# Kernel tuning notes

Hardware: AMD Instinct MI355X
Metric: run time of the kernel (lower is better)

The kernel has to match this reference:

```python
import jax, jax.numpy as jnp
import numpy as np

B, D, H, W, C = 2, 16, 16, 16, 64
CBAR = 32


def setup_inputs() -> dict:
    key = jax.random.key(0)
    ks = jax.random.split(key, 6)
    x = jax.random.normal(ks[0], (B, D, H, W, C), dtype=jnp.float32)
    # 1x1x1 Conv3D == per-voxel linear over channels; scale for stable softmax
    Wf = jax.random.normal(ks[1], (C, CBAR), dtype=jnp.float32) / np.sqrt(C)
    Wg = jax.random.normal(ks[2], (C, CBAR), dtype=jnp.float32) / np.sqrt(C)
    Wh = jax.random.normal(ks[3], (C, CBAR), dtype=jnp.float32) / np.sqrt(C)
    Wo = jax.random.normal(ks[4], (CBAR, C), dtype=jnp.float32) / np.sqrt(CBAR)
    bf = jnp.zeros((CBAR,), jnp.float32)
    bg = jnp.zeros((CBAR,), jnp.float32)
    bh = jnp.zeros((CBAR,), jnp.float32)
    bo = jnp.zeros((C,), jnp.float32)
    gamma = jnp.ones((), jnp.float32)
    return {"x": x, "Wf": Wf, "bf": bf, "Wg": Wg, "bg": bg,
            "Wh": Wh, "bh": bh, "Wo": Wo, "bo": bo, "gamma": gamma}


def reference(x, Wf, bf, Wg, bg, Wh, bh, Wo, bo, gamma):
    b, d, h, w, c = x.shape
    n = d * h * w
    xf = x.reshape(b, n, c)                       # [B, N, C]
    f = xf @ Wf + bf                              # [B, N, cbar] (keys)
    g = xf @ Wg + bg                              # [B, N, cbar] (queries)
    hv = xf @ Wh + bh                             # [B, N, cbar] (values)
    s = jnp.einsum('bqc,bkc->bqk', g, f)          # [B, N, N]
    beta = jax.nn.softmax(s, axis=-1)
    bhv = jnp.einsum('bqk,bkc->bqc', beta, hv)    # [B, N, cbar]
    o = bhv @ Wo + bo                             # [B, N, C]
    out = xf + gamma * o
    return out.reshape(b, d, h, w, c)
```

## Files before the change

kernel.cpp:

```cpp
#include <hip/hip_runtime.h>
#include <hip/hip_bf16.h>

typedef short short8 __attribute__((ext_vector_type(8)));
typedef float f32x4 __attribute__((ext_vector_type(4)));

__device__ __forceinline__ float bf2f(unsigned short v) {
    unsigned int u = ((unsigned int)v) << 16;
    float f;
    __builtin_memcpy(&f, &u, 4);
    return f;
}

__device__ __forceinline__ unsigned short f2bf(float f) {
    unsigned int u;
    __builtin_memcpy(&u, &f, 4);
    u += 0x7fffu + ((u >> 16) & 1u);
    return (unsigned short)(u >> 16);
}

__device__ __forceinline__ unsigned int pack2(float a, float b) {
    return (unsigned int)f2bf(a) | ((unsigned int)f2bf(b) << 16);
}

__device__ __forceinline__ unsigned int pack_trunc(float a, float b) {
    unsigned int ua, ub;
    __builtin_memcpy(&ua, &a, 4);
    __builtin_memcpy(&ub, &b, 4);
    return __builtin_amdgcn_perm(ub, ua, 0x07060302u);
}

__device__ __forceinline__ void split2(float a, float b,
                                       unsigned int& hi, unsigned int& lo) {
    unsigned short ah = f2bf(a), bh = f2bf(b);
    float al = a - bf2f(ah), bl = b - bf2f(bh);
    hi = (unsigned int)ah | ((unsigned int)bh << 16);
    lo = (unsigned int)f2bf(al) | ((unsigned int)f2bf(bl) << 16);
}

__device__ __forceinline__ float loadv(const void* p, int idx, bool is_fp32) {
    return is_fp32 ? ((const float*)p)[idx] : bf2f(((const unsigned short*)p)[idx]);
}
__device__ __forceinline__ bool detect_fp32(const void* x, int tid, int* flag_sh) {
    if (tid < 64) {
        unsigned int w = ((const unsigned int*)x)[tid];
        unsigned int e = (w >> 7) & 0xFFu;
        unsigned long long m = __ballot(e > 140u);
        if (tid == 0) *flag_sh = (__popcll(m) >= 8) ? 1 : 0;
    }
    __syncthreads();
    return *flag_sh != 0;
}

__global__ __launch_bounds__(128) void proj_kernel(
    const void* __restrict__ x,
    const void* __restrict__ Wf, const void* __restrict__ bfv,
    const void* __restrict__ Wg, const void* __restrict__ bgv,
    const void* __restrict__ Wh, const void* __restrict__ bhv,
    unsigned short* __restrict__ F, unsigned short* __restrict__ G,
    unsigned short* __restrict__ Ht) {
    __shared__ unsigned int WTh[3 * 32 * 36];
    __shared__ unsigned int WTl[3 * 32 * 36];
    __shared__ float bL[96];
    __shared__ int dflag;
    int tid = threadIdx.x;
    bool fp32 = detect_fp32(x, tid, &dflag);
    int lane = tid & 63, wave = tid >> 6;
    int Q = lane >> 4, l15 = lane & 15;
    int row0 = (blockIdx.x * 2 + wave) << 4;

    const void* Ws[3] = {Wf, Wg, Wh};
    const void* bs[3] = {bfv, bgv, bhv};

    for (int i = tid; i < 3072; i += 128) {
        int m = i >> 10;
        int r = i & 1023;
        int p = r >> 5, n = r & 31;
        float e0 = loadv(Ws[m], (2 * p) * 32 + n, fp32);
        float e1 = loadv(Ws[m], (2 * p + 1) * 32 + n, fp32);
        unsigned int hi, lo;
        split2(e0, e1, hi, lo);
        WTh[(m * 32 + n) * 36 + p] = hi;
        WTl[(m * 32 + n) * 36 + p] = lo;
    }
    if (tid < 96) bL[tid] = loadv(bs[tid >> 5], tid & 31, fp32);

    short8 a0h, a0l, a1h, a1l;
    {
        int base = (row0 + l15) * 64 + Q * 8;
        union { unsigned int u[4]; short8 s8; } A0h, A0l, A1h, A1l;
        if (fp32) {
            const float* xf = (const float*)x;
            f32x4 v0 = *(const f32x4*)(xf + base);
            f32x4 v1 = *(const f32x4*)(xf + base + 4);
            f32x4 w0 = *(const f32x4*)(xf + base + 32);
            f32x4 w1 = *(const f32x4*)(xf + base + 36);
            split2(v0[0], v0[1], A0h.u[0], A0l.u[0]);
            split2(v0[2], v0[3], A0h.u[1], A0l.u[1]);
            split2(v1[0], v1[1], A0h.u[2], A0l.u[2]);
            split2(v1[2], v1[3], A0h.u[3], A0l.u[3]);
            split2(w0[0], w0[1], A1h.u[0], A1l.u[0]);
            split2(w0[2], w0[3], A1h.u[1], A1l.u[1]);
            split2(w1[0], w1[1], A1h.u[2], A1l.u[2]);
            split2(w1[2], w1[3], A1h.u[3], A1l.u[3]);
        } else {
            const unsigned short* xb = (const unsigned short*)x;
            A0h.s8 = *(const short8*)(xb + base);
            A1h.s8 = *(const short8*)(xb + base + 32);
            A0l.u[0] = A0l.u[1] = A0l.u[2] = A0l.u[3] = 0;
            A1l = A0l;
        }
        a0h = A0h.s8; a0l = A0l.s8; a1h = A1h.s8; a1l = A1l.s8;
    }
    __syncthreads();

#pragma unroll
    for (int m = 0; m < 3; m++) {
#pragma unroll
        for (int cb = 0; cb < 2; cb++) {
            int rowbase = (m * 32 + cb * 16 + l15) * 36;
            union { uint4 v; short8 s8; } B0h, B0l, B1h, B1l;
            B0h.v = *(const uint4*)&WTh[rowbase + Q * 4];
            B1h.v = *(const uint4*)&WTh[rowbase + 16 + Q * 4];
            B0l.v = *(const uint4*)&WTl[rowbase + Q * 4];
            B1l.v = *(const uint4*)&WTl[rowbase + 16 + Q * 4];
            f32x4 z = {0.f, 0.f, 0.f, 0.f};
            f32x4 acc = __builtin_amdgcn_mfma_f32_16x16x32_bf16(a0h, B0h.s8, z, 0, 0, 0);
            acc = __builtin_amdgcn_mfma_f32_16x16x32_bf16(a0h, B0l.s8, acc, 0, 0, 0);
            acc = __builtin_amdgcn_mfma_f32_16x16x32_bf16(a0l, B0h.s8, acc, 0, 0, 0);
            acc = __builtin_amdgcn_mfma_f32_16x16x32_bf16(a1h, B1h.s8, acc, 0, 0, 0);
            acc = __builtin_amdgcn_mfma_f32_16x16x32_bf16(a1h, B1l.s8, acc, 0, 0, 0);
            acc = __builtin_amdgcn_mfma_f32_16x16x32_bf16(a1l, B1h.s8, acc, 0, 0, 0);
            float bias = bL[m * 32 + cb * 16 + l15];
            if (m < 2) {
                unsigned short* dst = (m == 0) ? F : G;
#pragma unroll
                for (int r = 0; r < 4; r++)
                    dst[(row0 + Q * 4 + r) * 32 + cb * 16 + l15] = f2bf(acc[r] + bias);
            } else {
                int b = row0 >> 12;
                int n0 = (row0 & 4095) + Q * 4;
                uint2 pk;
                pk.x = pack2(acc[0] + bias, acc[1] + bias);
                pk.y = pack2(acc[2] + bias, acc[3] + bias);
                *(uint2*)(Ht + b * 131072 + (cb * 16 + l15) * 4096 + n0) = pk;
            }
        }
    }
}

__global__ __launch_bounds__(512, 2) void attn_kernel(
    const unsigned short* __restrict__ F, const unsigned short* __restrict__ G,
    const unsigned short* __restrict__ Ht,
    const void* __restrict__ x,
    const void* __restrict__ Wo, const void* __restrict__ bo,
    const void* __restrict__ gamma_p,
    void* __restrict__ out) {
    __shared__ __attribute__((aligned(16))) unsigned short P_sh[8][2][16][40];
    __shared__ float O_lds[8][32][32];
    __shared__ float l_lds[8][32];
    __shared__ float Om[32][33];
    __shared__ float lmg[32];
    __shared__ float WoL[32][64];
    __shared__ float boL[64];
    __shared__ int dflag;

    int tid = threadIdx.x;
    bool fp32 = detect_fp32(x, tid, &dflag);

    for (int i = tid; i < 2048; i += 512) WoL[i >> 6][i & 63] = loadv(Wo, i, fp32);
    if (tid < 64) boL[tid] = loadv(bo, tid, fp32);

    int bx = blockIdx.x;
    int b = bx >> 7;
    int q0 = (bx & 127) << 5;
    int wave = tid >> 6;
    int lane = tid & 63;
    int Q = lane >> 4, l15 = lane & 15;

    const unsigned short* Fb = F + (b << 17);
    const unsigned short* Gb = G + (b << 17);
    const unsigned short* Htb = Ht + (b << 17);

    short8 g0 = *(const short8*)(Gb + ((q0 + l15) << 5) + (Q << 3));
    short8 g1 = *(const short8*)(Gb + ((q0 + 16 + l15) << 5) + (Q << 3));

    f32x4 O00 = {0.f, 0.f, 0.f, 0.f}, O01 = O00, O10 = O00, O11 = O00;
    float ls0 = 0.f, ls1 = 0.f;

    int k_begin = wave << 9;
    short8 af0 = *(const short8*)(Fb + ((k_begin + l15) << 5) + (Q << 3));
    short8 af1 = *(const short8*)(Fb + ((k_begin + 16 + l15) << 5) + (Q << 3));
    short8 bh0 = *(const short8*)(Htb + (l15 << 12) + k_begin + (Q << 3));
    short8 bh1 = *(const short8*)(Htb + ((16 + l15) << 12) + k_begin + (Q << 3));

    for (int it = 0; it < 16; ++it) {
        int itn = (it < 15) ? it + 1 : 15;
        int kn = k_begin + (itn << 5);
        short8 naf0 = *(const short8*)(Fb + ((kn + l15) << 5) + (Q << 3));
        short8 naf1 = *(const short8*)(Fb + ((kn + 16 + l15) << 5) + (Q << 3));
        short8 nbh0 = *(const short8*)(Htb + (l15 << 12) + kn + (Q << 3));
        short8 nbh1 = *(const short8*)(Htb + ((16 + l15) << 12) + kn + (Q << 3));

        f32x4 z = {0.f, 0.f, 0.f, 0.f};
        f32x4 c00 = __builtin_amdgcn_mfma_f32_16x16x32_bf16(af0, g0, z, 0, 0, 0);
        f32x4 c01 = __builtin_amdgcn_mfma_f32_16x16x32_bf16(af1, g0, z, 0, 0, 0);
        f32x4 c10 = __builtin_amdgcn_mfma_f32_16x16x32_bf16(af0, g1, z, 0, 0, 0);
        f32x4 c11 = __builtin_amdgcn_mfma_f32_16x16x32_bf16(af1, g1, z, 0, 0, 0);

        float e00[4], e01[4], e10[4], e11[4];
#pragma unroll
        for (int r = 0; r < 4; r++) {
            e00[r] = __expf(c00[r]); e01[r] = __expf(c01[r]);
            e10[r] = __expf(c10[r]); e11[r] = __expf(c11[r]);
            ls0 += e00[r] + e01[r];
            ls1 += e10[r] + e11[r];
        }

        uint2 w0, w1;
        w0.x = pack_trunc(e00[0], e00[1]); w0.y = pack_trunc(e00[2], e00[3]);
        w1.x = pack_trunc(e01[0], e01[1]); w1.y = pack_trunc(e01[2], e01[3]);
        *(uint2*)&P_sh[wave][0][l15][Q * 4] = w0;
        *(uint2*)&P_sh[wave][0][l15][16 + Q * 4] = w1;
        uint2 w2, w3;
        w2.x = pack_trunc(e10[0], e10[1]); w2.y = pack_trunc(e10[2], e10[3]);
        w3.x = pack_trunc(e11[0], e11[1]); w3.y = pack_trunc(e11[2], e11[3]);
        *(uint2*)&P_sh[wave][1][l15][Q * 4] = w2;
        *(uint2*)&P_sh[wave][1][l15][16 + Q * 4] = w3;

        short8 pf0 = *(const short8*)&P_sh[wave][0][l15][Q * 8];
        short8 pf1 = *(const short8*)&P_sh[wave][1][l15][Q * 8];

        O00 = __builtin_amdgcn_mfma_f32_16x16x32_bf16(pf0, bh0, O00, 0, 0, 0);
        O01 = __builtin_amdgcn_mfma_f32_16x16x32_bf16(pf0, bh1, O01, 0, 0, 0);
        O10 = __builtin_amdgcn_mfma_f32_16x16x32_bf16(pf1, bh0, O10, 0, 0, 0);
        O11 = __builtin_amdgcn_mfma_f32_16x16x32_bf16(pf1, bh1, O11, 0, 0, 0);

        af0 = naf0; af1 = naf1; bh0 = nbh0; bh1 = nbh1;
    }

    ls0 += __shfl_xor(ls0, 16); ls0 += __shfl_xor(ls0, 32);
    ls1 += __shfl_xor(ls1, 16); ls1 += __shfl_xor(ls1, 32);
    if (Q == 0) {
        l_lds[wave][l15] = ls0;
        l_lds[wave][16 + l15] = ls1;
    }
#pragma unroll
    for (int r = 0; r < 4; r++) {
        O_lds[wave][(Q << 2) | r][l15]             = O00[r];
        O_lds[wave][(Q << 2) | r][16 + l15]        = O01[r];
        O_lds[wave][16 + ((Q << 2) | r)][l15]      = O10[r];
        O_lds[wave][16 + ((Q << 2) | r)][16 + l15] = O11[r];
    }
    __syncthreads();

    if (tid < 32) {
        float s = 0.f;
#pragma unroll
        for (int w = 0; w < 8; w++) s += l_lds[w][tid];
        lmg[tid] = 1.0f / s;
    }
#pragma unroll
    for (int idx = tid; idx < 1024; idx += 512) {
        int q = idx >> 5, c = idx & 31;
        float s = 0.f;
#pragma unroll
        for (int w = 0; w < 8; w++) s += O_lds[w][q][c];
        Om[q][c] = s;
    }
    __syncthreads();

    int q = tid >> 4;
    int ch = (tid & 15) << 2;
    float a0 = 0.f, a1 = 0.f, a2 = 0.f, a3 = 0.f;
#pragma unroll
    for (int c = 0; c < 32; c++) {
        float ob = Om[q][c];
        f32x4 wr = *(const f32x4*)&WoL[c][ch];
        a0 += ob * wr[0]; a1 += ob * wr[1]; a2 += ob * wr[2]; a3 += ob * wr[3];
    }
    float inv = lmg[q];
    float gam = loadv(gamma_p, 0, fp32);
    int gq = q0 + q;
    int obase = (((b << 12) + gq) << 6) + ch;
    if (fp32) {
        f32x4 xv = *(const f32x4*)((const float*)x + obase);
        f32x4 ov;
        ov[0] = xv[0] + gam * (a0 * inv + boL[ch + 0]);
        ov[1] = xv[1] + gam * (a1 * inv + boL[ch + 1]);
        ov[2] = xv[2] + gam * (a2 * inv + boL[ch + 2]);
        ov[3] = xv[3] + gam * (a3 * inv + boL[ch + 3]);
        *(f32x4*)((float*)out + obase) = ov;
    } else {
        const unsigned short* xb = (const unsigned short*)x;
        unsigned short* ob16 = (unsigned short*)out;
        uint2 pk;
        pk.x = pack2(bf2f(xb[obase + 0]) + gam * (a0 * inv + boL[ch + 0]),
                     bf2f(xb[obase + 1]) + gam * (a1 * inv + boL[ch + 1]));
        pk.y = pack2(bf2f(xb[obase + 2]) + gam * (a2 * inv + boL[ch + 2]),
                     bf2f(xb[obase + 3]) + gam * (a3 * inv + boL[ch + 3]));
        *(uint2*)(ob16 + obase) = pk;
    }
}

extern "C" void kernel_launch(void* const* d_in, const int* in_sizes, int n_in,
                              void* d_out, int out_size, void* d_ws, size_t ws_size,
                              hipStream_t stream) {
    const void* x   = d_in[0];
    const void* Wf  = d_in[1];
    const void* bfv = d_in[2];
    const void* Wg  = d_in[3];
    const void* bgv = d_in[4];
    const void* Wh  = d_in[5];
    const void* bhv = d_in[6];
    const void* Wo  = d_in[7];
    const void* bo  = d_in[8];
    const void* gam = d_in[9];

    unsigned short* F  = (unsigned short*)d_ws;
    unsigned short* G  = F + 262144;
    unsigned short* Ht = G + 262144;

    proj_kernel<<<256, 128, 0, stream>>>(x, Wf, bfv, Wg, bgv, Wh, bhv, F, G, Ht);
    attn_kernel<<<256, 512, 0, stream>>>(F, G, Ht, x, Wo, bo, gam, d_out);
}
```

Before: 99.25 us.

## Use 16 waves per attention block and register shuffles for P fragments

Doubles the attention block to 1024 threads so each of 16 waves handles 256 keys instead of 512, splitting the key dimension further. The probability matrix is rearranged into MFMA A-fragment layout with cross-lane shuffles instead of a round trip through shared memory. Explicit software prefetch of the next F/Ht fragments is dropped in favour of unroll-by-2. The final reduction and output projection are remapped to 2 channels per thread. This adds a larger cross-wave reduction in LDS and more shuffle instructions, and may hurt occupancy and latency hiding.

Result: no change. 99.56 us (+0.3%).

```diff
diff --git a/kernel.cpp b/kernel.cpp
--- a/kernel.cpp
+++ b/kernel.cpp
@@ -49,6 +49,36 @@
     }
     __syncthreads();
     return *flag_sh != 0;
+}
+
+__device__ __forceinline__ short8 p_to_afrag(unsigned int pk0, unsigned int pk1,
+                                             unsigned int pk2, unsigned int pk3,
+                                             int lane) {
+    {
+        unsigned int s0 = __shfl_xor(pk0, 32), s2 = __shfl_xor(pk2, 32);
+        bool hi = (lane & 32) != 0;
+        unsigned int n0 = hi ? s2 : pk0;
+        unsigned int n2 = hi ? pk2 : s0;
+        pk0 = n0; pk2 = n2;
+        unsigned int s1 = __shfl_xor(pk1, 32), s3 = __shfl_xor(pk3, 32);
+        unsigned int n1 = hi ? s3 : pk1;
+        unsigned int n3 = hi ? pk3 : s1;
+        pk1 = n1; pk3 = n3;
+    }
+    {
+        unsigned int s0 = __shfl_xor(pk0, 16), s2 = __shfl_xor(pk2, 16);
+        bool hi = (lane & 16) != 0;
+        unsigned int n0 = hi ? s2 : pk0;
+        unsigned int n2 = hi ? pk2 : s0;
+        pk0 = n0; pk2 = n2;
+        unsigned int s1 = __shfl_xor(pk1, 16), s3 = __shfl_xor(pk3, 16);
+        unsigned int n1 = hi ? s3 : pk1;
+        unsigned int n3 = hi ? pk3 : s1;
+        pk1 = n1; pk3 = n3;
+    }
+    union { unsigned int u[4]; short8 s8; } pf;
+    pf.u[0] = pk0; pf.u[1] = pk1; pf.u[2] = pk2; pf.u[3] = pk3;
+    return pf.s8;
 }
 
 __global__ __launch_bounds__(128) void proj_kernel(
@@ -148,16 +178,15 @@
     }
 }
 
-__global__ __launch_bounds__(512, 2) void attn_kernel(
+__global__ __launch_bounds__(1024, 4) void attn_kernel(
     const unsigned short* __restrict__ F, const unsigned short* __restrict__ G,
     const unsigned short* __restrict__ Ht,
     const void* __restrict__ x,
     const void* __restrict__ Wo, const void* __restrict__ bo,
     const void* __restrict__ gamma_p,
     void* __restrict__ out) {
-    __shared__ __attribute__((aligned(16))) unsigned short P_sh[8][2][16][40];
-    __shared__ float O_lds[8][32][32];
-    __shared__ float l_lds[8][32];
+    __shared__ float O_lds[16][32][32];
+    __shared__ float l_lds[16][32];
     __shared__ float Om[32][33];
     __shared__ float lmg[32];
     __shared__ float WoL[32][64];
@@ -167,7 +196,7 @@
     int tid = threadIdx.x;
     bool fp32 = detect_fp32(x, tid, &dflag);
 
-    for (int i = tid; i < 2048; i += 512) WoL[i >> 6][i & 63] = loadv(Wo, i, fp32);
+    for (int i = tid; i < 2048; i += 1024) WoL[i >> 6][i & 63] = loadv(Wo, i, fp32);
     if (tid < 64) boL[tid] = loadv(bo, tid, fp32);
 
     int bx = blockIdx.x;
@@ -187,19 +216,14 @@
     f32x4 O00 = {0.f, 0.f, 0.f, 0.f}, O01 = O00, O10 = O00, O11 = O00;
     float ls0 = 0.f, ls1 = 0.f;
 
-    int k_begin = wave << 9;
-    short8 af0 = *(const short8*)(Fb + ((k_begin + l15) << 5) + (Q << 3));
-    short8 af1 = *(const short8*)(Fb + ((k_begin + 16 + l15) << 5) + (Q << 3));
-    short8 bh0 = *(const short8*)(Htb + (l15 << 12) + k_begin + (Q << 3));
-    short8 bh1 = *(const short8*)(Htb + ((16 + l15) << 12) + k_begin + (Q << 3));
-
-    for (int it = 0; it < 16; ++it) {
-        int itn = (it < 15) ? it + 1 : 15;
-        int kn = k_begin + (itn << 5);
-        short8 naf0 = *(const short8*)(Fb + ((kn + l15) << 5) + (Q << 3));
-        short8 naf1 = *(const short8*)(Fb + ((kn + 16 + l15) << 5) + (Q << 3));
-        short8 nbh0 = *(const short8*)(Htb + (l15 << 12) + kn + (Q << 3));
-        short8 nbh1 = *(const short8*)(Htb + ((16 + l15) << 12) + kn + (Q << 3));
+    int k_begin = wave << 8;
+#pragma unroll 2
+    for (int it = 0; it < 8; ++it) {
+        int kk = k_begin + (it << 5);
+        short8 af0 = *(const short8*)(Fb + ((kk + l15) << 5) + (Q << 3));
+        short8 af1 = *(const short8*)(Fb + ((kk + 16 + l15) << 5) + (Q << 3));
+        short8 bh0 = *(const short8*)(Htb + (l15 << 12) + kk + (Q << 3));
+        short8 bh1 = *(const short8*)(Htb + ((16 + l15) << 12) + kk + (Q << 3));
 
         f32x4 z = {0.f, 0.f, 0.f, 0.f};
         f32x4 c00 = __builtin_amdgcn_mfma_f32_16x16x32_bf16(af0, g0, z, 0, 0, 0);
@@ -216,26 +240,17 @@
             ls1 += e10[r] + e11[r];
         }
 
-        uint2 w0, w1;
-        w0.x = pack_trunc(e00[0], e00[1]); w0.y = pack_trunc(e00[2], e00[3]);
-        w1.x = pack_trunc(e01[0], e01[1]); w1.y = pack_trunc(e01[2], e01[3]);
-        *(uint2*)&P_sh[wave][0][l15][Q * 4] = w0;
-        *(uint2*)&P_sh[wave][0][l15][16 + Q * 4] = w1;
-        uint2 w2, w3;
-        w2.x = pack_trunc(e10[0], e10[1]); w2.y = pack_trunc(e10[2], e10[3]);
-        w3.x = pack_trunc(e11[0], e11[1]); w3.y = pack_trunc(e11[2], e11[3]);
-        *(uint2*)&P_sh[wave][1][l15][Q * 4] = w2;
-        *(uint2*)&P_sh[wave][1][l15][16 + Q * 4] = w3;
-
-        short8 pf0 = *(const short8*)&P_sh[wave][0][l15][Q * 8];
-        short8 pf1 = *(const short8*)&P_sh[wave][1][l15][Q * 8];
+        short8 pf0 = p_to_afrag(pack_trunc(e00[0], e00[1]), pack_trunc(e00[2], e00[3]),
+                                pack_trunc(e01[0], e01[1]), pack_trunc(e01[2], e01[3]),
+                                lane);
+        short8 pf1 = p_to_afrag(pack_trunc(e10[0], e10[1]), pack_trunc(e10[2], e10[3]),
+                                pack_trunc(e11[0], e11[1]), pack_trunc(e11[2], e11[3]),
+                                lane);
 
         O00 = __builtin_amdgcn_mfma_f32_16x16x32_bf16(pf0, bh0, O00, 0, 0, 0);
         O01 = __builtin_amdgcn_mfma_f32_16x16x32_bf16(pf0, bh1, O01, 0, 0, 0);
         O10 = __builtin_amdgcn_mfma_f32_16x16x32_bf16(pf1, bh0, O10, 0, 0, 0);
         O11 = __builtin_amdgcn_mfma_f32_16x16x32_bf16(pf1, bh1, O11, 0, 0, 0);
-
-        af0 = naf0; af1 = naf1; bh0 = nbh0; bh1 = nbh1;
     }
 
     ls0 += __shfl_xor(ls0, 16); ls0 += __shfl_xor(ls0, 32);
@@ -256,49 +271,43 @@
     if (tid < 32) {
         float s = 0.f;
 #pragma unroll
-        for (int w = 0; w < 8; w++) s += l_lds[w][tid];
+        for (int w = 0; w < 16; w++) s += l_lds[w][tid];
         lmg[tid] = 1.0f / s;
     }
-#pragma unroll
-    for (int idx = tid; idx < 1024; idx += 512) {
-        int q = idx >> 5, c = idx & 31;
+    {
+        int q = tid >> 5, c = tid & 31;
         float s = 0.f;
 #pragma unroll
-        for (int w = 0; w < 8; w++) s += O_lds[w][q][c];
+        for (int w = 0; w < 16; w++) s += O_lds[w][q][c];
         Om[q][c] = s;
     }
     __syncthreads();
 
-    int q = tid >> 4;
-    int ch = (tid & 15) << 2;
-    float a0 = 0.f, a1 = 0.f, a2 = 0.f, a3 = 0.f;
+    int q = tid >> 5;
+    int ch = (tid & 31) << 1;
+    float a0 = 0.f, a1 = 0.f;
 #pragma unroll
     for (int c = 0; c < 32; c++) {
         float ob = Om[q][c];
-        f32x4 wr = *(const f32x4*)&WoL[c][ch];
-        a0 += ob * wr[0]; a1 += ob * wr[1]; a2 += ob * wr[2]; a3 += ob * wr[3];
+        a0 += ob * WoL[c][ch];
+        a1 += ob * WoL[c][ch + 1];
     }
     float inv = lmg[q];
     float gam = loadv(gamma_p, 0, fp32);
     int gq = q0 + q;
     int obase = (((b << 12) + gq) << 6) + ch;
     if (fp32) {
-        f32x4 xv = *(const f32x4*)((const float*)x + obase);
-        f32x4 ov;
-        ov[0] = xv[0] + gam * (a0 * inv + boL[ch + 0]);
-        ov[1] = xv[1] + gam * (a1 * inv + boL[ch + 1]);
-        ov[2] = xv[2] + gam * (a2 * inv + boL[ch + 2]);
-        ov[3] = xv[3] + gam * (a3 * inv + boL[ch + 3]);
-        *(f32x4*)((float*)out + obase) = ov;
+        float2 xv = *(const float2*)((const float*)x + obase);
+        float2 ov;
+        ov.x = xv.x + gam * (a0 * inv + boL[ch + 0]);
+        ov.y = xv.y + gam * (a1 * inv + boL[ch + 1]);
+        *(float2*)((float*)out + obase) = ov;
     } else {
         const unsigned short* xb = (const unsigned short*)x;
         unsigned short* ob16 = (unsigned short*)out;
-        uint2 pk;
-        pk.x = pack2(bf2f(xb[obase + 0]) + gam * (a0 * inv + boL[ch + 0]),
-                     bf2f(xb[obase + 1]) + gam * (a1 * inv + boL[ch + 1]));
-        pk.y = pack2(bf2f(xb[obase + 2]) + gam * (a2 * inv + boL[ch + 2]),
-                     bf2f(xb[obase + 3]) + gam * (a3 * inv + boL[ch + 3]));
-        *(uint2*)(ob16 + obase) = pk;
+        unsigned int pk = pack2(bf2f(xb[obase + 0]) + gam * (a0 * inv + boL[ch + 0]),
+                                bf2f(xb[obase + 1]) + gam * (a1 * inv + boL[ch + 1]));
+        *(unsigned int*)(ob16 + obase) = pk;
     }
 }
 
@@ -321,5 +330,5 @@
     unsigned short* Ht = G + 262144;
 
     proj_kernel<<<256, 128, 0, stream>>>(x, Wf, bfv, Wg, bgv, Wh, bhv, F, G, Ht);
-    attn_kernel<<<256, 512, 0, stream>>>(F, G, Ht, x, Wo, bo, gam, d_out);
-}
+    attn_kernel<<<256, 1024, 0, stream>>>(F, G, Ht, x, Wo, bo, gam, d_out);
+}
```
